# Kernel tuning notes

Hardware: AMD Instinct MI355X
Metric: run time of the kernel (lower is better)

## Reference

```python
import jax, jax.numpy as jnp
import numpy as np

D = 768        # input_dim
H = 6          # num_heads
DH = D // H    # dim_head = 128
NQ = 512       # num_q (x seq len)
G = 64         # num_q_group
R = 64         # q_aware_to_v_lora_rank
MID = G * R    # all_q_mid = 4096
VREP = NQ // G # v_repeat = 8
EPS = 1e-5


def _ln(x, gamma, beta):
    mu = jnp.mean(x, axis=-1, keepdims=True)
    var = jnp.mean(jnp.square(x - mu), axis=-1, keepdims=True)
    return (x - mu) * jax.lax.rsqrt(var + EPS) * gamma + beta


def setup_inputs() -> dict:
    key = jax.random.key(0)
    ks = jax.random.split(key, 8)
    B, N = 4, 256
    s = 0.02
    return {
        "x": jax.random.normal(ks[0], (B, NQ, D), jnp.float32),
        "context": jax.random.normal(ks[1], (B, N, D), jnp.float32),
        "Wq": jax.random.normal(ks[2], (D, D), jnp.float32) * s,
        "gq": jnp.ones((D,), jnp.float32), "bq": jnp.zeros((D,), jnp.float32),
        "Wk": jax.random.normal(ks[3], (D, D), jnp.float32) * s,
        "gk": jnp.ones((D,), jnp.float32), "bk": jnp.zeros((D,), jnp.float32),
        "Wv1": jax.random.normal(ks[4], (D, MID), jnp.float32) * s,
        "gv1": jnp.ones((MID,), jnp.float32), "bv1": jnp.zeros((MID,), jnp.float32),
        "Wc": jax.random.normal(ks[5], (G, D, R), jnp.float32) * s,  # grouped 1x1 conv: per-group (R -> D)
        "gv2": jnp.ones((D,), jnp.float32), "bv2": jnp.zeros((D,), jnp.float32),
        "Wout": jax.random.normal(ks[6], (D, D), jnp.float32) * s,
    }


def reference(x, context, Wq, gq, bq, Wk, gk, bk, Wv1, gv1, bv1, Wc, gv2, bv2, Wout):
    B, _, _ = x.shape
    N = context.shape[1]
    # projections + LayerNorm (dropout is identity at eval)
    q = _ln(x @ Wq, gq, bq)                       # (B, NQ, D)
    k = _ln(context @ Wk, gk, bk)                 # (B, N, D)
    v1 = _ln(context @ Wv1, gv1, bv1)             # (B, N, MID)
    # grouped 1x1 conv: (B, N, G, R) x (G, D, R) -> (B, G, N, D)
    v1g = v1.reshape(B, N, G, R)
    v = jnp.einsum('bngr,gdr->bgnd', v1g, Wc)
    v = _ln(v, gv2, bv2)                          # (B, G, N, D)
    # split heads
    qh = q.reshape(B, NQ, H, DH).transpose(0, 2, 1, 3)        # (B, H, NQ, DH)
    kh = k.reshape(B, N, H, DH).transpose(0, 2, 1, 3)         # (B, H, N, DH)
    vh = v.reshape(B, G, N, H, DH).transpose(0, 3, 1, 2, 4)   # (B, H, G, N, DH)
    scale = DH ** (-0.25)
    sim = jnp.einsum('bhid,bhjd->bhij', qh * scale, kh * scale)
    attn = jax.nn.softmax(sim, axis=-1)                       # (B, H, NQ, N)
    # torch .repeat tiles the group dim: query i uses group (i % G).
    # reshape i -> (r, g) with i = r*G + g, avoiding materializing repeated v.
    attn_r = attn.reshape(B, H, VREP, G, N)
    out = jnp.einsum('bhrgj,bhgjd->bhrgd', attn_r, vh)        # (B, H, VREP, G, DH)
    out = out.reshape(B, H, NQ, DH).transpose(0, 2, 1, 3).reshape(B, NQ, D)
    return out @ Wout
```

## Files before the change

kernel.cpp:

```cpp
#include <hip/hip_runtime.h>
#include <cstddef>

#define B_ 4
#define NQ_ 512
#define N_ 256
#define D_ 768
#define H_ 6
#define DH_ 128
#define G_ 64
#define R_ 64
#define MID_ 4096
#define EPS_ 1e-5f
#define SCALE_ 0.29730177875068026f

typedef short bf16x8 __attribute__((ext_vector_type(8)));
typedef short short4v __attribute__((ext_vector_type(4)));
typedef float f32x4 __attribute__((ext_vector_type(4)));

__device__ __forceinline__ float b2f(short s) {
  union { float f; unsigned u; } c; c.u = ((unsigned)(unsigned short)s) << 16; return c.f;
}
__device__ __forceinline__ short f2b(float f) {
  union { float f; unsigned u; } c; c.f = f;
  unsigned r = c.u + 0x7FFFu + ((c.u >> 16) & 1u);
  return (short)(r >> 16);
}

#define AS1(p) ((const __attribute__((address_space(1))) unsigned int*)(p))
#define AS3(p) ((__attribute__((address_space(3))) unsigned int*)(p))

__global__ __launch_bounds__(256) void cast3_kernel(
    const float* __restrict__ x, short* __restrict__ xb,
    const float* __restrict__ ctx, short* __restrict__ cb,
    const float* __restrict__ Wc, short* __restrict__ Wcb) {
  int bid = blockIdx.x;
  const float* src; short* dst; int i;
  if (bid < 1536)      { src = x;   dst = xb;  i = (bid * 256 + threadIdx.x) * 4; }
  else if (bid < 2304) { src = ctx; dst = cb;  i = ((bid - 1536) * 256 + threadIdx.x) * 4; }
  else                 { src = Wc;  dst = Wcb; i = ((bid - 2304) * 256 + threadIdx.x) * 4; }
  float4 v = *(const float4*)&src[i];
  short4v o = {f2b(v.x), f2b(v.y), f2b(v.z), f2b(v.w)};
  *(short4v*)&dst[i] = o;
}

__device__ __forceinline__ void tcast_tile(const float* __restrict__ src,
                                           short* __restrict__ dst, int R, int C,
                                           int r0, int c0, float* tile ) {
  int t = threadIdx.x, tc = t & 31, tr = t >> 5;
#pragma unroll
  for (int i = 0; i < 4; ++i)
    tile[(tr + i * 8) * 33 + tc] = src[(size_t)(r0 + tr + i * 8) * C + c0 + tc];
  __syncthreads();
#pragma unroll
  for (int i = 0; i < 4; ++i)
    dst[(size_t)(c0 + tr + i * 8) * R + r0 + tc] = f2b(tile[tc * 33 + tr + i * 8]);
}

__global__ __launch_bounds__(256) void tcast4_kernel(
    const float* __restrict__ Wq, short* __restrict__ WqT,
    const float* __restrict__ Wk, short* __restrict__ WkT,
    const float* __restrict__ Wout, short* __restrict__ WoutT,
    const float* __restrict__ Wv1, short* __restrict__ Wv1T) {
  __shared__ float tile[32 * 33];
  int bid = blockIdx.x;
  if (bid < 576)       tcast_tile(Wq, WqT, 768, 768, (bid / 24) * 32, (bid % 24) * 32, tile);
  else if (bid < 1152) { int o = bid - 576;  tcast_tile(Wk, WkT, 768, 768, (o / 24) * 32, (o % 24) * 32, tile); }
  else if (bid < 1728) { int o = bid - 1152; tcast_tile(Wout, WoutT, 768, 768, (o / 24) * 32, (o % 24) * 32, tile); }
  else                 { int o = bid - 1728; tcast_tile(Wv1, Wv1T, 768, 4096, (o / 128) * 32, (o % 128) * 32, tile); }
}

__device__ __forceinline__ void gemm64_tile(
    const short* __restrict__ A, const short* __restrict__ BT,
    float* __restrict__ C, int N, int K, int m0, int n0,
    short* As , short* Bs ) {
  int t = threadIdx.x, w = t >> 6, l = t & 63;
  int lr = l & 15, hi = l >> 4, lk = hi * 8;
  int wr = (w >> 1) * 64, wc = (w & 1) * 32;
  f32x4 acc[4][2];
#pragma unroll
  for (int i = 0; i < 4; ++i)
#pragma unroll
    for (int j = 0; j < 2; ++j) acc[i][j] = (f32x4)0.f;
  const short* Ap = A + (size_t)(m0 + (t >> 2)) * K + (t & 3) * 8;
  const short* Bp = BT + (size_t)(n0 + (t >> 2)) * K + (t & 3) * 8;
  for (int k0 = 0; k0 < K; k0 += 32) {
    __builtin_amdgcn_global_load_lds(AS1(Ap + k0), AS3(&As[w * 512]), 16, 0, 0);
    __builtin_amdgcn_global_load_lds(AS1(Ap + (size_t)64 * K + k0), AS3(&As[2048 + w * 512]), 16, 0, 0);
    __builtin_amdgcn_global_load_lds(AS1(Bp + k0), AS3(&Bs[w * 512]), 16, 0, 0);
    __syncthreads();
    bf16x8 af[4], bfr[2];
#pragma unroll
    for (int mi = 0; mi < 4; ++mi) af[mi] = *(const bf16x8*)&As[(wr + mi * 16 + lr) * 32 + lk];
#pragma unroll
    for (int ni = 0; ni < 2; ++ni) bfr[ni] = *(const bf16x8*)&Bs[(wc + ni * 16 + lr) * 32 + lk];
#pragma unroll
    for (int mi = 0; mi < 4; ++mi)
#pragma unroll
      for (int ni = 0; ni < 2; ++ni)
        acc[mi][ni] = __builtin_amdgcn_mfma_f32_16x16x32_bf16(af[mi], bfr[ni], acc[mi][ni], 0, 0, 0);
    __syncthreads();
  }
#pragma unroll
  for (int mi = 0; mi < 4; ++mi)
#pragma unroll
    for (int ni = 0; ni < 2; ++ni)
#pragma unroll
      for (int r = 0; r < 4; ++r)
        C[(size_t)(m0 + wr + mi * 16 + hi * 4 + r) * N + n0 + wc + ni * 16 + lr] = acc[mi][ni][r];
}

__global__ __launch_bounds__(256, 2) void proj_gemm_kernel(
    const short* __restrict__ xb, const short* __restrict__ WqT, float* __restrict__ tq,
    const short* __restrict__ cb, const short* __restrict__ WkT, float* __restrict__ tk,
    const short* __restrict__ Wv1T, float* __restrict__ tv) {
  __shared__ __align__(16) short As[128 * 32];
  __shared__ __align__(16) short Bs[64 * 32];
  int bid = blockIdx.x;
  if (bid < 192)      gemm64_tile(xb, WqT, tq, 768, 768, (bid / 12) * 128, (bid % 12) * 64, As, Bs);
  else if (bid < 288) { int o = bid - 192; gemm64_tile(cb, WkT, tk, 768, 768, (o / 12) * 128, (o % 12) * 64, As, Bs); }
  else                { int o = bid - 288; gemm64_tile(cb, Wv1T, tv, 4096, 768, (o / 64) * 128, (o % 64) * 64, As, Bs); }
}

__global__ __launch_bounds__(256, 2) void out_gemm_kernel(
    const short* __restrict__ aoutb, const short* __restrict__ WoutT, float* __restrict__ C) {
  __shared__ __align__(16) short As[128 * 32];
  __shared__ __align__(16) short Bs[64 * 32];
  int bid = blockIdx.x;
  gemm64_tile(aoutb, WoutT, C, 768, 768, (bid / 12) * 128, (bid % 12) * 64, As, Bs);
}

__global__ __launch_bounds__(256) void ln_all_kernel(
    const float* __restrict__ tq, const float* __restrict__ tk, const float* __restrict__ tv,
    const float* __restrict__ gq, const float* __restrict__ bq,
    const float* __restrict__ gk, const float* __restrict__ bk,
    const float* __restrict__ gv1, const float* __restrict__ bv1,
    short* __restrict__ qb, short* __restrict__ kb, short* __restrict__ v1b) {
  __shared__ float reds[4], redq[4];
  int row = blockIdx.x, t = threadIdx.x;
  const float* src; const float* gamma; const float* beta; int C; float scale;
  if (row < 2048)      { src = tq + (size_t)row * 768; gamma = gq; beta = bq; C = 768; scale = SCALE_; }
  else if (row < 3072) { src = tk + (size_t)(row - 2048) * 768; gamma = gk; beta = bk; C = 768; scale = SCALE_; }
  else                 { src = tv + (size_t)(row - 3072) * 4096; gamma = gv1; beta = bv1; C = 4096; scale = 1.f; }
  float s = 0.f, q2 = 0.f;
  for (int c = t; c < C; c += 256) { float v = src[c]; s += v; q2 += v * v; }
#pragma unroll
  for (int off = 32; off; off >>= 1) { s += __shfl_down(s, off); q2 += __shfl_down(q2, off); }
  int w = t >> 6;
  if ((t & 63) == 0) { reds[w] = s; redq[w] = q2; }
  __syncthreads();
  s = reds[0] + reds[1] + reds[2] + reds[3];
  q2 = redq[0] + redq[1] + redq[2] + redq[3];
  float mu = s / C, var = q2 / C - mu * mu;
  float rstd = rsqrtf(var + EPS_);
  if (row < 2048) {
    for (int c = t; c < C; c += 256)
      qb[(size_t)row * 768 + c] = f2b(((src[c] - mu) * rstd * gamma[c] + beta[c]) * scale);
  } else if (row < 3072) {
    int rr = row - 2048, b = rr >> 8, j = rr & 255;
    for (int c = t; c < C; c += 256) {
      short val = f2b(((src[c] - mu) * rstd * gamma[c] + beta[c]) * scale);
      kb[((size_t)((b * H_ + (c >> 7)) * N_ + j)) * DH_ + (c & 127)] = val;
    }
  } else {
    int rr = row - 3072;
    for (int c = t; c < C; c += 256)
      v1b[(size_t)rr * MID_ + c] = f2b((src[c] - mu) * rstd * gamma[c] + beta[c]);
  }
}

__global__ __launch_bounds__(256, 2) void attn_mfma_kernel(
    const short* __restrict__ qb, const short* __restrict__ kb, short* __restrict__ Ps) {
  int b = blockIdx.z, h = blockIdx.y, i0 = blockIdx.x * 64;
  int t = threadIdx.x, w = t >> 6, l = t & 63;
  int lr = l & 15, hi = l >> 4;
  bf16x8 af[4];
  const short* qp = qb + ((size_t)(b * NQ_ + i0 + w * 16 + lr)) * D_ + h * DH_ + hi * 8;
#pragma unroll
  for (int kk = 0; kk < 4; ++kk) af[kk] = *(const bf16x8*)(qp + kk * 32);
  f32x4 acc[16];
#pragma unroll
  for (int jf = 0; jf < 16; ++jf) acc[jf] = (f32x4)0.f;
  const short* kp = kb + ((size_t)((b * H_ + h) * N_ + lr)) * DH_ + hi * 8;
#pragma unroll
  for (int kk = 0; kk < 4; ++kk)
#pragma unroll
    for (int jf = 0; jf < 16; ++jf) {
      bf16x8 bfr = *(const bf16x8*)(kp + jf * 16 * DH_ + kk * 32);
      acc[jf] = __builtin_amdgcn_mfma_f32_16x16x32_bf16(af[kk], bfr, acc[jf], 0, 0, 0);
    }
  float mx[4], sum[4];
#pragma unroll
  for (int r = 0; r < 4; ++r) {
    mx[r] = acc[0][r];
#pragma unroll
    for (int jf = 1; jf < 16; ++jf) mx[r] = fmaxf(mx[r], acc[jf][r]);
  }
#pragma unroll
  for (int off = 1; off < 16; off <<= 1)
#pragma unroll
    for (int r = 0; r < 4; ++r) mx[r] = fmaxf(mx[r], __shfl_xor(mx[r], off));
#pragma unroll
  for (int r = 0; r < 4; ++r) sum[r] = 0.f;
#pragma unroll
  for (int jf = 0; jf < 16; ++jf)
#pragma unroll
    for (int r = 0; r < 4; ++r) {
      float p = __expf(acc[jf][r] - mx[r]);
      acc[jf][r] = p; sum[r] += p;
    }
#pragma unroll
  for (int off = 1; off < 16; off <<= 1)
#pragma unroll
    for (int r = 0; r < 4; ++r) sum[r] += __shfl_xor(sum[r], off);
  float inv[4];
#pragma unroll
  for (int r = 0; r < 4; ++r) inv[r] = 1.f / sum[r];
  short* pp = Ps + ((size_t)((b * H_ + h) * NQ_ + i0 + w * 16 + hi * 4)) * N_ + lr;
#pragma unroll
  for (int jf = 0; jf < 16; ++jf)
#pragma unroll
    for (int r = 0; r < 4; ++r)
      pp[(size_t)r * N_ + jf * 16] = f2b(acc[jf][r] * inv[r]);
}

__global__ __launch_bounds__(512, 2) void pv_mfma_kernel(
    const short* __restrict__ v1b, const short* __restrict__ Wcb,
    const short* __restrict__ Ps, const float* __restrict__ gv2,
    const float* __restrict__ bv2, short* __restrict__ aoutb) {
  __shared__ __align__(16) short V1s[256 * 72];
  __shared__ __align__(16) short Wcs[128 * 72];
  __shared__ __align__(16) short Ls[128 * 256];
  __shared__ __align__(16) short As2[56 * 256];
  __shared__ float mean_s[256], rstd_s[256];
  int bg = blockIdx.x, b = bg >> 6, g = bg & 63;
  int t = threadIdx.x, w = t >> 6, l = t & 63;
  int lr = l & 15, hi = l >> 4, lk = hi * 8;

#pragma unroll
  for (int it = 0; it < 4; ++it) {
    int idx = it * 512 + t;
    int n = idx >> 3, seg = (idx & 7) * 8;
    *(bf16x8*)&V1s[n * 72 + seg] =
        *(const bf16x8*)&v1b[((size_t)(b * N_ + n)) * MID_ + g * R_ + seg];
  }
#pragma unroll
  for (int it = 0; it < 6; ++it) {
    int e = it * 512 + t;
    int i = e >> 6, q4 = e & 63;
    short4v v = *(const short4v*)&Ps[((size_t)((b * H_ + (i >> 3)) * NQ_ + (i & 7) * G_ + g)) * N_ + q4 * 4];
    int phys = (((q4 >> 1) ^ ((i & 7) << 2)) << 4) | ((q4 & 1) << 3);
    *(short4v*)((char*)&As2[i * 256] + phys) = v;
  }
  {
    short4v z = {0, 0, 0, 0};
    *(short4v*)&As2[48 * 256 + t * 4] = z;
  }

  float sum_[2][4], sq_[2][4];
#pragma unroll
  for (int mi = 0; mi < 2; ++mi)
#pragma unroll
    for (int r = 0; r < 4; ++r) { sum_[mi][r] = 0.f; sq_[mi][r] = 0.f; }

  for (int ci = 0; ci < 6; ++ci) {
#pragma unroll
    for (int it = 0; it < 2; ++it) {
      int e = it * 512 + t;
      int dd = e >> 3, seg = (e & 7) * 8;
      *(bf16x8*)&Wcs[dd * 72 + seg] =
          *(const bf16x8*)&Wcb[((size_t)(g * D_ + ci * 128 + dd)) * R_ + seg];
    }
    __syncthreads();
#pragma unroll
    for (int nb = 0; nb < 2; ++nb) {
      f32x4 cacc[2][4];
#pragma unroll
      for (int mi = 0; mi < 2; ++mi)
#pragma unroll
        for (int nj = 0; nj < 4; ++nj) cacc[mi][nj] = (f32x4)0.f;
#pragma unroll
      for (int k0 = 0; k0 < 64; k0 += 32) {
        bf16x8 a0 = *(const bf16x8*)&V1s[(w * 32 + lr) * 72 + k0 + lk];
        bf16x8 a1 = *(const bf16x8*)&V1s[(w * 32 + 16 + lr) * 72 + k0 + lk];
#pragma unroll
        for (int nj = 0; nj < 4; ++nj) {
          bf16x8 bfr = *(const bf16x8*)&Wcs[((nb * 4 + nj) * 16 + lr) * 72 + k0 + lk];
          cacc[0][nj] = __builtin_amdgcn_mfma_f32_16x16x32_bf16(a0, bfr, cacc[0][nj], 0, 0, 0);
          cacc[1][nj] = __builtin_amdgcn_mfma_f32_16x16x32_bf16(a1, bfr, cacc[1][nj], 0, 0, 0);
        }
      }
#pragma unroll
      for (int mi = 0; mi < 2; ++mi)
#pragma unroll
        for (int nj = 0; nj < 4; ++nj) {
          f32x4 c = cacc[mi][nj];
#pragma unroll
          for (int r = 0; r < 4; ++r) { sum_[mi][r] += c[r]; sq_[mi][r] += c[r] * c[r]; }
        }
    }
    __syncthreads();
  }
#pragma unroll
  for (int off = 1; off < 16; off <<= 1)
#pragma unroll
    for (int mi = 0; mi < 2; ++mi)
#pragma unroll
      for (int r = 0; r < 4; ++r) {
        sum_[mi][r] += __shfl_xor(sum_[mi][r], off);
        sq_[mi][r] += __shfl_xor(sq_[mi][r], off);
      }
  if (lr == 0) {
#pragma unroll
    for (int mi = 0; mi < 2; ++mi)
#pragma unroll
      for (int r = 0; r < 4; ++r) {
        int n = w * 32 + mi * 16 + hi * 4 + r;
        float mu = sum_[mi][r] * (1.f / 768.f);
        float var = sq_[mi][r] * (1.f / 768.f) - mu * mu;
        mean_s[n] = mu;
        rstd_s[n] = rsqrtf(var + EPS_);
      }
  }

#pragma unroll
  for (int it = 0; it < 2; ++it) {
    int e = it * 512 + t;
    int dd = e >> 3, seg = (e & 7) * 8;
    *(bf16x8*)&Wcs[dd * 72 + seg] = *(const bf16x8*)&Wcb[((size_t)(g * D_ + dd)) * R_ + seg];
  }
  __syncthreads();

  for (int ci = 0; ci < 6; ++ci) {
    int d0 = ci * 128;
    f32x4 cacc[2][8];
#pragma unroll
    for (int mi = 0; mi < 2; ++mi)
#pragma unroll
      for (int ni = 0; ni < 8; ++ni) cacc[mi][ni] = (f32x4)0.f;
#pragma unroll
    for (int k0 = 0; k0 < 64; k0 += 32) {
      bf16x8 a0 = *(const bf16x8*)&V1s[(w * 32 + lr) * 72 + k0 + lk];
      bf16x8 a1 = *(const bf16x8*)&V1s[(w * 32 + 16 + lr) * 72 + k0 + lk];
#pragma unroll
      for (int ni = 0; ni < 8; ++ni) {
        bf16x8 bfr = *(const bf16x8*)&Wcs[(ni * 16 + lr) * 72 + k0 + lk];
        cacc[0][ni] = __builtin_amdgcn_mfma_f32_16x16x32_bf16(a0, bfr, cacc[0][ni], 0, 0, 0);
        cacc[1][ni] = __builtin_amdgcn_mfma_f32_16x16x32_bf16(a1, bfr, cacc[1][ni], 0, 0, 0);
      }
    }
    float mn[2][4], rs[2][4];
#pragma unroll
    for (int mi = 0; mi < 2; ++mi)
#pragma unroll
      for (int r = 0; r < 4; ++r) {
        int nrow = w * 32 + mi * 16 + hi * 4 + r;
        mn[mi][r] = mean_s[nrow];
        rs[mi][r] = rstd_s[nrow];
      }
    float gc[8], bc[8];
#pragma unroll
    for (int ni = 0; ni < 8; ++ni) {
      gc[ni] = gv2[d0 + ni * 16 + lr];
      bc[ni] = bv2[d0 + ni * 16 + lr];
    }
#pragma unroll
    for (int mi = 0; mi < 2; ++mi)
#pragma unroll
      for (int ni = 0; ni < 8; ++ni) {
        f32x4 c = cacc[mi][ni];
        short4v o = {f2b((c[0] - mn[mi][0]) * rs[mi][0] * gc[ni] + bc[ni]),
                     f2b((c[1] - mn[mi][1]) * rs[mi][1] * gc[ni] + bc[ni]),
                     f2b((c[2] - mn[mi][2]) * rs[mi][2] * gc[ni] + bc[ni]),
                     f2b((c[3] - mn[mi][3]) * rs[mi][3] * gc[ni] + bc[ni])};
        int row = ni * 16 + lr;
        int bcol = w * 64 + mi * 32 + hi * 8;
        int phys = (((bcol >> 4) ^ ((lr & 7) << 2)) << 4) | (bcol & 15);
        *(short4v*)((char*)&Ls[row * 256] + phys) = o;
      }
    __syncthreads();

    f32x4 acc2 = (f32x4)0.f;
#pragma unroll
    for (int k0 = 0; k0 < 256; k0 += 32) {
      int physoff = ((((k0 >> 3) + hi) ^ ((lr & 7) << 2)) << 4);
      bf16x8 pa = *(const bf16x8*)((char*)&As2[(ci * 8 + lr) * 256] + physoff);
      bf16x8 pb = *(const bf16x8*)((char*)&Ls[(w * 16 + lr) * 256] + physoff);
      acc2 = __builtin_amdgcn_mfma_f32_16x16x32_bf16(pa, pb, acc2, 0, 0, 0);
    }
    if (ci < 5) {
#pragma unroll
      for (int it = 0; it < 2; ++it) {
        int e = it * 512 + t;
        int dd = e >> 3, seg = (e & 7) * 8;
        *(bf16x8*)&Wcs[dd * 72 + seg] =
            *(const bf16x8*)&Wcb[((size_t)(g * D_ + d0 + 128 + dd)) * R_ + seg];
      }
    }
    if (hi < 2) {
      int dcol = d0 + w * 16 + lr;
#pragma unroll
      for (int r = 0; r < 4; ++r) {
        int rr = hi * 4 + r;
        aoutb[((size_t)(b * NQ_ + rr * G_ + g)) * D_ + dcol] = f2b(acc2[r]);
      }
    }
    __syncthreads();
  }
}

extern "C" void kernel_launch(void* const* d_in, const int* in_sizes, int n_in,
                              void* d_out, int out_size, void* d_ws, size_t ws_size,
                              hipStream_t stream) {
  const float* x       = (const float*)d_in[0];
  const float* context = (const float*)d_in[1];
  const float* Wq  = (const float*)d_in[2];
  const float* gq  = (const float*)d_in[3];
  const float* bq  = (const float*)d_in[4];
  const float* Wk  = (const float*)d_in[5];
  const float* gk  = (const float*)d_in[6];
  const float* bk  = (const float*)d_in[7];
  const float* Wv1 = (const float*)d_in[8];
  const float* gv1 = (const float*)d_in[9];
  const float* bv1 = (const float*)d_in[10];
  const float* Wc  = (const float*)d_in[11];
  const float* gv2 = (const float*)d_in[12];
  const float* bv2 = (const float*)d_in[13];
  const float* Wout = (const float*)d_in[14];
  float* out = (float*)d_out;

  char* p = (char*)d_ws;
  float* tq   = (float*)p; p += (size_t)1572864 * 4;
  float* tk   = (float*)p; p += (size_t)786432 * 4;
  float* tv   = (float*)p; p += (size_t)4194304 * 4;
  short* xb   = (short*)p; p += (size_t)1572864 * 2;
  short* cb   = (short*)p; p += (size_t)786432 * 2;
  short* WqT  = (short*)p; p += (size_t)589824 * 2;
  short* WkT  = (short*)p; p += (size_t)589824 * 2;
  short* Wv1T = (short*)p; p += (size_t)3145728 * 2;
  short* WoutT= (short*)p; p += (size_t)589824 * 2;
  short* Wcb  = (short*)p; p += (size_t)3145728 * 2;
  short* qb   = (short*)p; p += (size_t)1572864 * 2;
  short* kb   = (short*)p; p += (size_t)786432 * 2;
  short* v1b  = (short*)p; p += (size_t)4194304 * 2;
  short* Ps   = (short*)p; p += (size_t)3145728 * 2;
  short* aoutb= (short*)p; p += (size_t)1572864 * 2;

  dim3 blk(256);
  cast3_kernel<<<5376, blk, 0, stream>>>(x, xb, context, cb, Wc, Wcb);
  tcast4_kernel<<<4800, blk, 0, stream>>>(Wq, WqT, Wk, WkT, Wout, WoutT, Wv1, Wv1T);
  proj_gemm_kernel<<<800, blk, 0, stream>>>(xb, WqT, tq, cb, WkT, tk, Wv1T, tv);
  ln_all_kernel<<<4096, blk, 0, stream>>>(tq, tk, tv, gq, bq, gk, bk, gv1, bv1, qb, kb, v1b);
  attn_mfma_kernel<<<dim3(8, H_, B_), blk, 0, stream>>>(qb, kb, Ps);
  pv_mfma_kernel<<<B_ * G_, dim3(512), 0, stream>>>(v1b, Wcb, Ps, gv2, bv2, aoutb);
  out_gemm_kernel<<<192, blk, 0, stream>>>(aoutb, WoutT, out);
}
```

Before: 211.4 us.

## Compute second LayerNorm stats via precomputed Wc Gram matrix instead of full conv pass

Precomputes, per group, the Gram matrix Wc^T Wc and the column sums of Wc in a new weight-prep kernel. The pv kernel then gets each row's mean and variance for the grouped-conv LayerNorm from a small 64x65 MFMA product with v1, rather than running the full 768-wide conv once just to collect statistics. The cast and transpose-cast kernels are merged into one launch with wider vector accesses, ln_all holds row values in registers, and the LDS swizzle is replaced by row padding. This costs extra workspace and a weight-only preprocessing kernel each call, and the statistics now come from bf16-rounded Gram sums, which could affect accuracy.

```diff
diff --git a/kernel.cpp b/kernel.cpp
--- a/kernel.cpp
+++ b/kernel.cpp
@@ -29,44 +29,79 @@
 #define AS1(p) ((const __attribute__((address_space(1))) unsigned int*)(p))
 #define AS3(p) ((__attribute__((address_space(3))) unsigned int*)(p))
 
-__global__ __launch_bounds__(256) void cast3_kernel(
+__global__ __launch_bounds__(256) void prep_kernel(
     const float* __restrict__ x, short* __restrict__ xb,
     const float* __restrict__ ctx, short* __restrict__ cb,
-    const float* __restrict__ Wc, short* __restrict__ Wcb) {
-  int bid = blockIdx.x;
-  const float* src; short* dst; int i;
-  if (bid < 1536)      { src = x;   dst = xb;  i = (bid * 256 + threadIdx.x) * 4; }
-  else if (bid < 2304) { src = ctx; dst = cb;  i = ((bid - 1536) * 256 + threadIdx.x) * 4; }
-  else                 { src = Wc;  dst = Wcb; i = ((bid - 2304) * 256 + threadIdx.x) * 4; }
-  float4 v = *(const float4*)&src[i];
-  short4v o = {f2b(v.x), f2b(v.y), f2b(v.z), f2b(v.w)};
-  *(short4v*)&dst[i] = o;
-}
-
-__device__ __forceinline__ void tcast_tile(const float* __restrict__ src,
-                                           short* __restrict__ dst, int R, int C,
-                                           int r0, int c0, float* tile ) {
-  int t = threadIdx.x, tc = t & 31, tr = t >> 5;
-#pragma unroll
-  for (int i = 0; i < 4; ++i)
-    tile[(tr + i * 8) * 33 + tc] = src[(size_t)(r0 + tr + i * 8) * C + c0 + tc];
-  __syncthreads();
-#pragma unroll
-  for (int i = 0; i < 4; ++i)
-    dst[(size_t)(c0 + tr + i * 8) * R + r0 + tc] = f2b(tile[tc * 33 + tr + i * 8]);
-}
-
-__global__ __launch_bounds__(256) void tcast4_kernel(
+    const float* __restrict__ Wc, short* __restrict__ Wcb,
     const float* __restrict__ Wq, short* __restrict__ WqT,
     const float* __restrict__ Wk, short* __restrict__ WkT,
     const float* __restrict__ Wout, short* __restrict__ WoutT,
     const float* __restrict__ Wv1, short* __restrict__ Wv1T) {
-  __shared__ float tile[32 * 33];
-  int bid = blockIdx.x;
-  if (bid < 576)       tcast_tile(Wq, WqT, 768, 768, (bid / 24) * 32, (bid % 24) * 32, tile);
-  else if (bid < 1152) { int o = bid - 576;  tcast_tile(Wk, WkT, 768, 768, (o / 24) * 32, (o % 24) * 32, tile); }
-  else if (bid < 1728) { int o = bid - 1152; tcast_tile(Wout, WoutT, 768, 768, (o / 24) * 32, (o % 24) * 32, tile); }
-  else                 { int o = bid - 1728; tcast_tile(Wv1, Wv1T, 768, 4096, (o / 128) * 32, (o % 128) * 32, tile); }
+  __shared__ float tile[64 * 65];
+  int bid = blockIdx.x, t = threadIdx.x;
+  if (bid < 2688) {
+    const float* src; short* dst; size_t i;
+    if (bid < 768)       { src = x;   dst = xb;  i = ((size_t)bid * 256 + t) * 8; }
+    else if (bid < 1152) { src = ctx; dst = cb;  i = ((size_t)(bid - 768) * 256 + t) * 8; }
+    else                 { src = Wc;  dst = Wcb; i = ((size_t)(bid - 1152) * 256 + t) * 8; }
+    float4 a = *(const float4*)&src[i], b = *(const float4*)&src[i + 4];
+    bf16x8 o = {f2b(a.x), f2b(a.y), f2b(a.z), f2b(a.w),
+                f2b(b.x), f2b(b.y), f2b(b.z), f2b(b.w)};
+    *(bf16x8*)&dst[i] = o;
+    return;
+  }
+  const float* src; short* dst; int R, C, o;
+  if (bid < 2832)      { src = Wq;   dst = WqT;   R = 768; C = 768;  o = bid - 2688; }
+  else if (bid < 2976) { src = Wk;   dst = WkT;   R = 768; C = 768;  o = bid - 2832; }
+  else if (bid < 3120) { src = Wout; dst = WoutT; R = 768; C = 768;  o = bid - 2976; }
+  else                 { src = Wv1;  dst = Wv1T;  R = 768; C = 4096; o = bid - 3120; }
+  int nct = C >> 6;
+  int tr0 = (o / nct) * 64, tc0 = (o % nct) * 64;
+  int rl = t >> 4, cl = (t & 15) * 4;
+#pragma unroll
+  for (int i = 0; i < 4; ++i) {
+    float4 v = *(const float4*)&src[(size_t)(tr0 + rl + i * 16) * C + tc0 + cl];
+    float* tp = &tile[(rl + i * 16) * 65 + cl];
+    tp[0] = v.x; tp[1] = v.y; tp[2] = v.z; tp[3] = v.w;
+  }
+  __syncthreads();
+#pragma unroll
+  for (int i = 0; i < 4; ++i) {
+    int c = rl + i * 16;
+    short4v ov = {f2b(tile[(cl + 0) * 65 + c]), f2b(tile[(cl + 1) * 65 + c]),
+                  f2b(tile[(cl + 2) * 65 + c]), f2b(tile[(cl + 3) * 65 + c])};
+    *(short4v*)&dst[(size_t)(tc0 + c) * R + tr0 + cl] = ov;
+  }
+}
+
+__global__ __launch_bounds__(256) void wprep_kernel(
+    const short* __restrict__ Wcb, float* __restrict__ Msum4, float* __restrict__ wcsum4) {
+  __shared__ __align__(16) float wd[16][64];
+  int g = blockIdx.x >> 2, qq = blockIdx.x & 3, t = threadIdx.x;
+  int r1 = t >> 2, r2b = (t & 3) * 16;
+  float acc[16] = {};
+  float wsum = 0.f;
+  const short* base = Wcb + ((size_t)g * D_ + qq * 192) * R_;
+  for (int d0 = 0; d0 < 192; d0 += 16) {
+    for (int idx = t; idx < 1024; idx += 256)
+      wd[idx >> 6][idx & 63] = b2f(base[(size_t)(d0 + (idx >> 6)) * R_ + (idx & 63)]);
+    __syncthreads();
+#pragma unroll 4
+    for (int i = 0; i < 16; ++i) {
+      float a = wd[i][r1];
+#pragma unroll
+      for (int kk = 0; kk < 16; ++kk) acc[kk] += a * wd[i][r2b + kk];
+    }
+    if (t < 64) {
+#pragma unroll 4
+      for (int i = 0; i < 16; ++i) wsum += wd[i][t];
+    }
+    __syncthreads();
+  }
+  float* mp = Msum4 + ((size_t)(qq * 64 + g)) * 4096;
+#pragma unroll
+  for (int kk = 0; kk < 16; ++kk) mp[r1 * 64 + r2b + kk] = acc[kk];
+  if (t < 64) wcsum4[(qq * 64 + g) * 64 + t] = wsum;
 }
 
 __device__ __forceinline__ void gemm64_tile(
@@ -137,34 +172,58 @@
     short* __restrict__ qb, short* __restrict__ kb, short* __restrict__ v1b) {
   __shared__ float reds[4], redq[4];
   int row = blockIdx.x, t = threadIdx.x;
-  const float* src; const float* gamma; const float* beta; int C; float scale;
-  if (row < 2048)      { src = tq + (size_t)row * 768; gamma = gq; beta = bq; C = 768; scale = SCALE_; }
-  else if (row < 3072) { src = tk + (size_t)(row - 2048) * 768; gamma = gk; beta = bk; C = 768; scale = SCALE_; }
-  else                 { src = tv + (size_t)(row - 3072) * 4096; gamma = gv1; beta = bv1; C = 4096; scale = 1.f; }
-  float s = 0.f, q2 = 0.f;
-  for (int c = t; c < C; c += 256) { float v = src[c]; s += v; q2 += v * v; }
-#pragma unroll
-  for (int off = 32; off; off >>= 1) { s += __shfl_down(s, off); q2 += __shfl_down(q2, off); }
-  int w = t >> 6;
-  if ((t & 63) == 0) { reds[w] = s; redq[w] = q2; }
-  __syncthreads();
-  s = reds[0] + reds[1] + reds[2] + reds[3];
-  q2 = redq[0] + redq[1] + redq[2] + redq[3];
-  float mu = s / C, var = q2 / C - mu * mu;
-  float rstd = rsqrtf(var + EPS_);
-  if (row < 2048) {
-    for (int c = t; c < C; c += 256)
-      qb[(size_t)row * 768 + c] = f2b(((src[c] - mu) * rstd * gamma[c] + beta[c]) * scale);
-  } else if (row < 3072) {
-    int rr = row - 2048, b = rr >> 8, j = rr & 255;
-    for (int c = t; c < C; c += 256) {
-      short val = f2b(((src[c] - mu) * rstd * gamma[c] + beta[c]) * scale);
-      kb[((size_t)((b * H_ + (c >> 7)) * N_ + j)) * DH_ + (c & 127)] = val;
+  int wv = t >> 6;
+  if (row < 3072) {
+    const float* src; const float* gamma; const float* beta;
+    if (row < 2048) { src = tq + (size_t)row * 768; gamma = gq; beta = bq; }
+    else            { src = tk + (size_t)(row - 2048) * 768; gamma = gk; beta = bk; }
+    float v0 = src[t], v1 = src[t + 256], v2 = src[t + 512];
+    float s = v0 + v1 + v2, q2 = v0 * v0 + v1 * v1 + v2 * v2;
+#pragma unroll
+    for (int off = 32; off; off >>= 1) { s += __shfl_down(s, off); q2 += __shfl_down(q2, off); }
+    if ((t & 63) == 0) { reds[wv] = s; redq[wv] = q2; }
+    __syncthreads();
+    s = reds[0] + reds[1] + reds[2] + reds[3];
+    q2 = redq[0] + redq[1] + redq[2] + redq[3];
+    float mu = s * (1.f / 768.f), var = q2 * (1.f / 768.f) - mu * mu;
+    float rstd = rsqrtf(var + EPS_);
+    float o0 = ((v0 - mu) * rstd * gamma[t] + beta[t]) * SCALE_;
+    float o1 = ((v1 - mu) * rstd * gamma[t + 256] + beta[t + 256]) * SCALE_;
+    float o2 = ((v2 - mu) * rstd * gamma[t + 512] + beta[t + 512]) * SCALE_;
+    if (row < 2048) {
+      qb[(size_t)row * 768 + t] = f2b(o0);
+      qb[(size_t)row * 768 + t + 256] = f2b(o1);
+      qb[(size_t)row * 768 + t + 512] = f2b(o2);
+    } else {
+      int rr = row - 2048, b = rr >> 8, j = rr & 255;
+      int c0 = t, c1 = t + 256, c2 = t + 512;
+      kb[((size_t)((b * H_ + (c0 >> 7)) * N_ + j)) * DH_ + (c0 & 127)] = f2b(o0);
+      kb[((size_t)((b * H_ + (c1 >> 7)) * N_ + j)) * DH_ + (c1 & 127)] = f2b(o1);
+      kb[((size_t)((b * H_ + (c2 >> 7)) * N_ + j)) * DH_ + (c2 & 127)] = f2b(o2);
     }
   } else {
     int rr = row - 3072;
-    for (int c = t; c < C; c += 256)
-      v1b[(size_t)rr * MID_ + c] = f2b((src[c] - mu) * rstd * gamma[c] + beta[c]);
+    const float* src = tv + (size_t)rr * 4096;
+    float vals[16];
+    float s = 0.f, q2 = 0.f;
+#pragma unroll
+    for (int p = 0; p < 16; ++p) {
+      vals[p] = src[t + p * 256];
+      s += vals[p]; q2 += vals[p] * vals[p];
+    }
+#pragma unroll
+    for (int off = 32; off; off >>= 1) { s += __shfl_down(s, off); q2 += __shfl_down(q2, off); }
+    if ((t & 63) == 0) { reds[wv] = s; redq[wv] = q2; }
+    __syncthreads();
+    s = reds[0] + reds[1] + reds[2] + reds[3];
+    q2 = redq[0] + redq[1] + redq[2] + redq[3];
+    float mu = s * (1.f / 4096.f), var = q2 * (1.f / 4096.f) - mu * mu;
+    float rstd = rsqrtf(var + EPS_);
+#pragma unroll
+    for (int p = 0; p < 16; ++p) {
+      int c = t + p * 256;
+      v1b[(size_t)rr * 4096 + c] = f2b((vals[p] - mu) * rstd * gv1[c] + bv1[c]);
+    }
   }
 }
 
@@ -223,18 +282,21 @@
       pp[(size_t)r * N_ + jf * 16] = f2b(acc[jf][r] * inv[r]);
 }
 
-__global__ __launch_bounds__(512, 2) void pv_mfma_kernel(
+#define LLS 264
+__global__ __launch_bounds__(512, 1) void pv_mfma_kernel(
     const short* __restrict__ v1b, const short* __restrict__ Wcb,
-    const short* __restrict__ Ps, const float* __restrict__ gv2,
+    const short* __restrict__ Ps, const float* __restrict__ Msum4,
+    const float* __restrict__ wcsum4, const float* __restrict__ gv2,
     const float* __restrict__ bv2, short* __restrict__ aoutb) {
   __shared__ __align__(16) short V1s[256 * 72];
   __shared__ __align__(16) short Wcs[128 * 72];
-  __shared__ __align__(16) short Ls[128 * 256];
-  __shared__ __align__(16) short As2[56 * 256];
+  __shared__ __align__(16) short Ls[128 * LLS];
+  __shared__ __align__(16) short As2[56 * LLS];
   __shared__ float mean_s[256], rstd_s[256];
   int bg = blockIdx.x, b = bg >> 6, g = bg & 63;
   int t = threadIdx.x, w = t >> 6, l = t & 63;
   int lr = l & 15, hi = l >> 4, lk = hi * 8;
+  short* MsB = Ls;
 
 #pragma unroll
   for (int it = 0; it < 4; ++it) {
@@ -243,85 +305,82 @@
     *(bf16x8*)&V1s[n * 72 + seg] =
         *(const bf16x8*)&v1b[((size_t)(b * N_ + n)) * MID_ + g * R_ + seg];
   }
+  for (int idx = t; idx < 65 * 64; idx += 512) {
+    int rho = idx >> 6, r = idx & 63;
+    float v;
+    if (rho < 64)
+      v = Msum4[(size_t)g * 4096 + rho * 64 + r] + Msum4[(size_t)(64 + g) * 4096 + rho * 64 + r] +
+          Msum4[(size_t)(128 + g) * 4096 + rho * 64 + r] + Msum4[(size_t)(192 + g) * 4096 + rho * 64 + r];
+    else
+      v = wcsum4[g * 64 + r] + wcsum4[(64 + g) * 64 + r] +
+          wcsum4[(128 + g) * 64 + r] + wcsum4[(192 + g) * 64 + r];
+    MsB[rho * 72 + r] = f2b(v * (1.f / 768.f));
+  }
 #pragma unroll
   for (int it = 0; it < 6; ++it) {
-    int e = it * 512 + t;
-    int i = e >> 6, q4 = e & 63;
-    short4v v = *(const short4v*)&Ps[((size_t)((b * H_ + (i >> 3)) * NQ_ + (i & 7) * G_ + g)) * N_ + q4 * 4];
-    int phys = (((q4 >> 1) ^ ((i & 7) << 2)) << 4) | ((q4 & 1) << 3);
-    *(short4v*)((char*)&As2[i * 256] + phys) = v;
-  }
+    int idx = it * 512 + t;
+    int i = idx >> 6, c4 = idx & 63;
+    short4v v = *(const short4v*)&Ps[((size_t)((b * H_ + (i >> 3)) * NQ_ + (i & 7) * G_ + g)) * N_ + c4 * 4];
+    *(short4v*)&As2[i * LLS + c4 * 4] = v;
+  }
+  for (int idx = t; idx < 528; idx += 512) {
+    short4v z = {0, 0, 0, 0};
+    *(short4v*)&As2[48 * LLS + idx * 4] = z;
+  }
+  __syncthreads();
+
   {
-    short4v z = {0, 0, 0, 0};
-    *(short4v*)&As2[48 * 256 + t * 4] = z;
-  }
-
-  float sum_[2][4], sq_[2][4];
-#pragma unroll
-  for (int mi = 0; mi < 2; ++mi)
-#pragma unroll
-    for (int r = 0; r < 4; ++r) { sum_[mi][r] = 0.f; sq_[mi][r] = 0.f; }
-
-  for (int ci = 0; ci < 6; ++ci) {
-#pragma unroll
-    for (int it = 0; it < 2; ++it) {
-      int e = it * 512 + t;
-      int dd = e >> 3, seg = (e & 7) * 8;
-      *(bf16x8*)&Wcs[dd * 72 + seg] =
-          *(const bf16x8*)&Wcb[((size_t)(g * D_ + ci * 128 + dd)) * R_ + seg];
-    }
-    __syncthreads();
-#pragma unroll
-    for (int nb = 0; nb < 2; ++nb) {
-      f32x4 cacc[2][4];
+    f32x4 sacc[2][5];
+#pragma unroll
+    for (int mi = 0; mi < 2; ++mi)
+#pragma unroll
+      for (int nj = 0; nj < 5; ++nj) sacc[mi][nj] = (f32x4)0.f;
+#pragma unroll
+    for (int k0 = 0; k0 < 64; k0 += 32) {
+      bf16x8 a0 = *(const bf16x8*)&V1s[(w * 32 + lr) * 72 + k0 + lk];
+      bf16x8 a1 = *(const bf16x8*)&V1s[(w * 32 + 16 + lr) * 72 + k0 + lk];
+#pragma unroll
+      for (int nj = 0; nj < 5; ++nj) {
+        bf16x8 bfr = *(const bf16x8*)&MsB[(nj * 16 + lr) * 72 + k0 + lk];
+        sacc[0][nj] = __builtin_amdgcn_mfma_f32_16x16x32_bf16(a0, bfr, sacc[0][nj], 0, 0, 0);
+        sacc[1][nj] = __builtin_amdgcn_mfma_f32_16x16x32_bf16(a1, bfr, sacc[1][nj], 0, 0, 0);
+      }
+    }
+    float pmsq[2][4], pmean[2][4];
+#pragma unroll
+    for (int mi = 0; mi < 2; ++mi)
+#pragma unroll
+      for (int j = 0; j < 4; ++j) {
+        int n = w * 32 + mi * 16 + hi * 4 + j;
+        float s = 0.f;
+#pragma unroll
+        for (int nj = 0; nj < 4; ++nj)
+          s += sacc[mi][nj][j] * b2f(V1s[n * 72 + nj * 16 + lr]);
+        pmsq[mi][j] = s;
+        pmean[mi][j] = (lr == 0) ? sacc[mi][4][j] : 0.f;
+      }
+#pragma unroll
+    for (int off = 1; off < 16; off <<= 1)
 #pragma unroll
       for (int mi = 0; mi < 2; ++mi)
 #pragma unroll
-        for (int nj = 0; nj < 4; ++nj) cacc[mi][nj] = (f32x4)0.f;
-#pragma unroll
-      for (int k0 = 0; k0 < 64; k0 += 32) {
-        bf16x8 a0 = *(const bf16x8*)&V1s[(w * 32 + lr) * 72 + k0 + lk];
-        bf16x8 a1 = *(const bf16x8*)&V1s[(w * 32 + 16 + lr) * 72 + k0 + lk];
-#pragma unroll
-        for (int nj = 0; nj < 4; ++nj) {
-          bf16x8 bfr = *(const bf16x8*)&Wcs[((nb * 4 + nj) * 16 + lr) * 72 + k0 + lk];
-          cacc[0][nj] = __builtin_amdgcn_mfma_f32_16x16x32_bf16(a0, bfr, cacc[0][nj], 0, 0, 0);
-          cacc[1][nj] = __builtin_amdgcn_mfma_f32_16x16x32_bf16(a1, bfr, cacc[1][nj], 0, 0, 0);
+        for (int j = 0; j < 4; ++j) {
+          pmsq[mi][j] += __shfl_xor(pmsq[mi][j], off);
+          pmean[mi][j] += __shfl_xor(pmean[mi][j], off);
         }
-      }
+    if (lr == 0) {
 #pragma unroll
       for (int mi = 0; mi < 2; ++mi)
 #pragma unroll
-        for (int nj = 0; nj < 4; ++nj) {
-          f32x4 c = cacc[mi][nj];
-#pragma unroll
-          for (int r = 0; r < 4; ++r) { sum_[mi][r] += c[r]; sq_[mi][r] += c[r] * c[r]; }
+        for (int j = 0; j < 4; ++j) {
+          int n = w * 32 + mi * 16 + hi * 4 + j;
+          float mu = pmean[mi][j];
+          float var = pmsq[mi][j] - mu * mu;
+          mean_s[n] = mu;
+          rstd_s[n] = rsqrtf(var + EPS_);
         }
     }
-    __syncthreads();
-  }
-#pragma unroll
-  for (int off = 1; off < 16; off <<= 1)
-#pragma unroll
-    for (int mi = 0; mi < 2; ++mi)
-#pragma unroll
-      for (int r = 0; r < 4; ++r) {
-        sum_[mi][r] += __shfl_xor(sum_[mi][r], off);
-        sq_[mi][r] += __shfl_xor(sq_[mi][r], off);
-      }
-  if (lr == 0) {
-#pragma unroll
-    for (int mi = 0; mi < 2; ++mi)
-#pragma unroll
-      for (int r = 0; r < 4; ++r) {
-        int n = w * 32 + mi * 16 + hi * 4 + r;
-        float mu = sum_[mi][r] * (1.f / 768.f);
-        float var = sq_[mi][r] * (1.f / 768.f) - mu * mu;
-        mean_s[n] = mu;
-        rstd_s[n] = rsqrtf(var + EPS_);
-      }
-  }
-
+  }
 #pragma unroll
   for (int it = 0; it < 2; ++it) {
     int e = it * 512 + t;
@@ -368,23 +427,19 @@
 #pragma unroll
       for (int ni = 0; ni < 8; ++ni) {
         f32x4 c = cacc[mi][ni];
-        short4v o = {f2b((c[0] - mn[mi][0]) * rs[mi][0] * gc[ni] + bc[ni]),
-                     f2b((c[1] - mn[mi][1]) * rs[mi][1] * gc[ni] + bc[ni]),
-                     f2b((c[2] - mn[mi][2]) * rs[mi][2] * gc[ni] + bc[ni]),
-                     f2b((c[3] - mn[mi][3]) * rs[mi][3] * gc[ni] + bc[ni])};
-        int row = ni * 16 + lr;
-        int bcol = w * 64 + mi * 32 + hi * 8;
-        int phys = (((bcol >> 4) ^ ((lr & 7) << 2)) << 4) | (bcol & 15);
-        *(short4v*)((char*)&Ls[row * 256] + phys) = o;
+        short4v ov = {f2b((c[0] - mn[mi][0]) * rs[mi][0] * gc[ni] + bc[ni]),
+                      f2b((c[1] - mn[mi][1]) * rs[mi][1] * gc[ni] + bc[ni]),
+                      f2b((c[2] - mn[mi][2]) * rs[mi][2] * gc[ni] + bc[ni]),
+                      f2b((c[3] - mn[mi][3]) * rs[mi][3] * gc[ni] + bc[ni])};
+        *(short4v*)&Ls[(ni * 16 + lr) * LLS + w * 32 + mi * 16 + hi * 4] = ov;
       }
     __syncthreads();
 
     f32x4 acc2 = (f32x4)0.f;
 #pragma unroll
     for (int k0 = 0; k0 < 256; k0 += 32) {
-      int physoff = ((((k0 >> 3) + hi) ^ ((lr & 7) << 2)) << 4);
-      bf16x8 pa = *(const bf16x8*)((char*)&As2[(ci * 8 + lr) * 256] + physoff);
-      bf16x8 pb = *(const bf16x8*)((char*)&Ls[(w * 16 + lr) * 256] + physoff);
+      bf16x8 pa = *(const bf16x8*)&As2[(ci * 8 + lr) * LLS + k0 + lk];
+      bf16x8 pb = *(const bf16x8*)&Ls[(w * 16 + lr) * LLS + k0 + lk];
       acc2 = __builtin_amdgcn_mfma_f32_16x16x32_bf16(pa, pb, acc2, 0, 0, 0);
     }
     if (ci < 5) {
@@ -429,28 +484,31 @@
   float* out = (float*)d_out;
 
   char* p = (char*)d_ws;
-  float* tq   = (float*)p; p += (size_t)1572864 * 4;
-  float* tk   = (float*)p; p += (size_t)786432 * 4;
-  float* tv   = (float*)p; p += (size_t)4194304 * 4;
-  short* xb   = (short*)p; p += (size_t)1572864 * 2;
-  short* cb   = (short*)p; p += (size_t)786432 * 2;
-  short* WqT  = (short*)p; p += (size_t)589824 * 2;
-  short* WkT  = (short*)p; p += (size_t)589824 * 2;
-  short* Wv1T = (short*)p; p += (size_t)3145728 * 2;
-  short* WoutT= (short*)p; p += (size_t)589824 * 2;
-  short* Wcb  = (short*)p; p += (size_t)3145728 * 2;
-  short* qb   = (short*)p; p += (size_t)1572864 * 2;
-  short* kb   = (short*)p; p += (size_t)786432 * 2;
-  short* v1b  = (short*)p; p += (size_t)4194304 * 2;
-  short* Ps   = (short*)p; p += (size_t)3145728 * 2;
-  short* aoutb= (short*)p; p += (size_t)1572864 * 2;
+  float* tq    = (float*)p; p += (size_t)1572864 * 4;
+  float* tk    = (float*)p; p += (size_t)786432 * 4;
+  float* tv    = (float*)p; p += (size_t)4194304 * 4;
+  float* Msum4 = (float*)p; p += (size_t)1048576 * 4;
+  float* wcsum4= (float*)p; p += (size_t)16384 * 4;
+  short* xb    = (short*)p; p += (size_t)1572864 * 2;
+  short* cb    = (short*)p; p += (size_t)786432 * 2;
+  short* WqT   = (short*)p; p += (size_t)589824 * 2;
+  short* WkT   = (short*)p; p += (size_t)589824 * 2;
+  short* Wv1T  = (short*)p; p += (size_t)3145728 * 2;
+  short* WoutT = (short*)p; p += (size_t)589824 * 2;
+  short* Wcb   = (short*)p; p += (size_t)3145728 * 2;
+  short* qb    = (short*)p; p += (size_t)1572864 * 2;
+  short* kb    = (short*)p; p += (size_t)786432 * 2;
+  short* v1b   = (short*)p; p += (size_t)4194304 * 2;
+  short* Ps    = (short*)p; p += (size_t)3145728 * 2;
+  short* aoutb = (short*)p; p += (size_t)1572864 * 2;
 
   dim3 blk(256);
-  cast3_kernel<<<5376, blk, 0, stream>>>(x, xb, context, cb, Wc, Wcb);
-  tcast4_kernel<<<4800, blk, 0, stream>>>(Wq, WqT, Wk, WkT, Wout, WoutT, Wv1, Wv1T);
+  prep_kernel<<<3888, blk, 0, stream>>>(x, xb, context, cb, Wc, Wcb,
+                                        Wq, WqT, Wk, WkT, Wout, WoutT, Wv1, Wv1T);
+  wprep_kernel<<<256, blk, 0, stream>>>(Wcb, Msum4, wcsum4);
   proj_gemm_kernel<<<800, blk, 0, stream>>>(xb, WqT, tq, cb, WkT, tk, Wv1T, tv);
   ln_all_kernel<<<4096, blk, 0, stream>>>(tq, tk, tv, gq, bq, gk, bk, gv1, bv1, qb, kb, v1b);
   attn_mfma_kernel<<<dim3(8, H_, B_), blk, 0, stream>>>(qb, kb, Ps);
-  pv_mfma_kernel<<<B_ * G_, dim3(512), 0, stream>>>(v1b, Wcb, Ps, gv2, bv2, aoutb);
+  pv_mfma_kernel<<<B_ * G_, dim3(512), 0, stream>>>(v1b, Wcb, Ps, Msum4, wcsum4, gv2, bv2, aoutb);
   out_gemm_kernel<<<192, blk, 0, stream>>>(aoutb, WoutT, out);
 }
```

After: 233.9 us. 10.6% more time.
